# Kernel optimization log

Measured on AMD Instinct MI355X. Metric: run time of the kernel, lower is better.

## Reference

```python
import jax, jax.numpy as jnp
import numpy as np

N_NODES = 50000
N_EDGES = 800000
N_GRAPHS = 512


def gcn_conv(x, W, b, src, dst, n_nodes):
    # Standard PyG GCNConv: linear transform, add self-loops, D^-1/2 (A+I) D^-1/2 aggregation.
    x = x @ W  # [N, out]
    loop = jnp.arange(n_nodes, dtype=src.dtype)
    s = jnp.concatenate([src, loop])  # [E+N]
    d = jnp.concatenate([dst, loop])
    deg = jax.ops.segment_sum(jnp.ones_like(d, dtype=x.dtype), d, num_segments=n_nodes)
    dinv = jnp.where(deg > 0, jax.lax.rsqrt(jnp.maximum(deg, 1e-12)), 0.0)
    norm = dinv[s] * dinv[d]  # [E+N]
    msg = x[s] * norm[:, None]  # gather + scale
    out = jax.ops.segment_sum(msg, d, num_segments=n_nodes)  # scatter-add
    return out + b


def setup_inputs() -> dict:
    key = jax.random.key(0)
    ks = jax.random.split(key, 10)
    x = jax.random.normal(ks[0], (N_NODES, 128), dtype=jnp.float32)
    edge_index = jax.random.randint(ks[1], (2, N_EDGES), 0, N_NODES, dtype=jnp.int64)
    batch = jnp.sort(jax.random.randint(ks[2], (N_NODES,), 0, N_GRAPHS, dtype=jnp.int64))
    y = jax.random.randint(ks[3], (N_GRAPHS,), 0, 4, dtype=jnp.int64)
    W1 = jax.random.normal(ks[4], (128, 64), dtype=jnp.float32) * (1.0 / np.sqrt(128))
    b1 = jnp.zeros((64,), dtype=jnp.float32)
    W2 = jax.random.normal(ks[5], (64, 64), dtype=jnp.float32) * (1.0 / np.sqrt(64))
    b2 = jnp.zeros((64,), dtype=jnp.float32)
    Wfc = jax.random.normal(ks[6], (64, 4), dtype=jnp.float32) * (1.0 / np.sqrt(64))
    bfc = jnp.zeros((4,), dtype=jnp.float32)
    return {"x": x, "edge_index": edge_index, "batch": batch, "y": y,
            "W1": W1, "b1": b1, "W2": W2, "b2": b2, "Wfc": Wfc, "bfc": bfc}


def reference(x, edge_index, batch, y, W1, b1, W2, b2, Wfc, bfc):
    src, dst = edge_index[0], edge_index[1]
    h = jax.nn.relu(gcn_conv(x, W1, b1, src, dst, N_NODES))
    h = jax.nn.relu(gcn_conv(h, W2, b2, src, dst, N_NODES))
    # global mean pool over graph ids
    sums = jax.ops.segment_sum(h, batch, num_segments=N_GRAPHS)  # [G, out]
    cnts = jax.ops.segment_sum(jnp.ones((h.shape[0],), h.dtype), batch, num_segments=N_GRAPHS)
    pooled = sums / jnp.maximum(cnts, 1.0)[:, None]
    logits = pooled @ Wfc + bfc
    logp = jax.nn.log_softmax(logits, axis=1)
    return (logp, y)
```

## Files before the change

### kernel.cpp

```cpp
#include <hip/hip_runtime.h>
#include <hip/hip_fp16.h>
#include <math.h>

#define N_NODES 50000
#define N_EDGES 800000
#define N_GRAPHS 512
#define NBKT 196
#define SENT N_NODES
#define CAP_T 6144
#define CAP_S 8192

typedef float v2f __attribute__((ext_vector_type(2)));

#define OFF_BCNT    0u
#define OFF_DINV    1024u
#define OFF_OFFS2   201216u
#define OFF_TMP     601344u
#define OFF_SORTED  5418240u
#define OFF_XS8_1   11840768u
#define OFF_XS8_2   15041024u
#define OFF_H2      18241280u

__global__ __launch_bounds__(256) void binA(const int* __restrict__ src, const int* __restrict__ dst,
                                            int* __restrict__ bcnt, unsigned int* __restrict__ tmp,
                                            unsigned int* __restrict__ x1, unsigned int* __restrict__ x2) {
    __shared__ int cnt[256];
    __shared__ int lo[256];
    __shared__ int cnt2[256];
    __shared__ int baseg[256];
    __shared__ unsigned int ldsPK[4096];
    __shared__ int ldsDST[4096];
    int t = threadIdx.x;
    cnt[t] = 0; cnt2[t] = 0;
    if (blockIdx.x == 0) {
        if (t < 16) x1[N_NODES * 16 + t] = 0;
        else if (t < 32) x2[N_NODES * 16 + (t - 16)] = 0;
    }
    __syncthreads();
    int e0 = blockIdx.x * 4096;
    int nE = N_EDGES - e0; if (nE > 4096) nE = 4096;
    int sA[16], dA[16];
#pragma unroll
    for (int i = 0; i < 16; ++i) {
        int e = e0 + i * 256 + t;
        if (e < N_EDGES) {
            sA[i] = src[e];
            dA[i] = dst[e];
            atomicAdd(&cnt[dA[i] >> 8], 1);
        } else dA[i] = -1;
    }
    __syncthreads();
    {
        int v = cnt[t];
        lo[t] = v;
        __syncthreads();
        for (int d = 1; d < 256; d <<= 1) {
            int a = (t >= d) ? lo[t - d] : 0;
            __syncthreads();
            lo[t] += a;
            __syncthreads();
        }
        int ex = lo[t] - v;
        __syncthreads();
        lo[t] = ex;
        baseg[t] = (t < NBKT && v) ? atomicAdd(&bcnt[t], v) : 0;
    }
    __syncthreads();
#pragma unroll
    for (int i = 0; i < 16; ++i) {
        if (dA[i] >= 0) {
            int b = dA[i] >> 8;
            int pl = lo[b] + atomicAdd(&cnt2[b], 1);
            ldsPK[pl] = (unsigned int)sA[i] | ((unsigned int)(dA[i] & 255) << 17);
            ldsDST[pl] = b * CAP_T + baseg[b] + (pl - lo[b]);
        }
    }
    __syncthreads();
    for (int p = t; p < nE; p += 256)
        tmp[ldsDST[p]] = ldsPK[p];
}

__global__ __launch_bounds__(256) void binB2(const unsigned int* __restrict__ tmp,
                                             const int* __restrict__ bcnt,
                                             int* __restrict__ sorted, int2* __restrict__ offs2,
                                             float* __restrict__ dinv) {
    __shared__ int cnt[256];
    __shared__ int scn[256];
    __shared__ int cur[256];
    __shared__ int ldsS[CAP_S];
    int b = blockIdx.x, t = threadIdx.x;
    cnt[t] = 0;
    __syncthreads();
    int m = bcnt[b];
    const unsigned int* tp = tmp + b * CAP_T;
    for (int e = t; e < m; e += 256) atomicAdd(&cnt[tp[e] >> 17], 1);
    __syncthreads();
    int deg = cnt[t];
    int pdeg = (deg + 7) & ~7;
    scn[t] = pdeg;
    __syncthreads();
    for (int d = 1; d < 256; d <<= 1) {
        int a = (t >= d) ? scn[t - d] : 0;
        __syncthreads();
        scn[t] += a;
        __syncthreads();
    }
    int begl = scn[t] - pdeg;
    int ptot = scn[255];
    int node = b * 256 + t;
    if (node < N_NODES) {
        offs2[node] = make_int2(b * CAP_S + begl, b * CAP_S + begl + pdeg);
        dinv[node] = rsqrtf(1.0f + (float)deg);
    }
    cur[t] = begl;
    __syncthreads();
    for (int e = t; e < m; e += 256) {
        unsigned int pk = tp[e];
        int p = atomicAdd(&cur[pk >> 17], 1);
        ldsS[p] = (int)(pk & 0x1FFFFu);
    }
    __syncthreads();
    for (int p = cur[t]; p < begl + pdeg; ++p) ldsS[p] = SENT;
    __syncthreads();
    int4* dst4 = (int4*)(sorted + b * CAP_S);
    const int4* src4 = (const int4*)ldsS;
    for (int p = t; p < (ptot >> 2); p += 256) dst4[p] = src4[p];
}

__global__ __launch_bounds__(256) void gemm1(const float* __restrict__ X, const float* __restrict__ W,
                                             const float* __restrict__ dinv, unsigned int* __restrict__ xs8) {
    __shared__ float sW[128 * 64];
    __shared__ float sX[16 * 132];
    int tid = threadIdx.x;
    {
        const float4* ws = (const float4*)W;
        float4* wd = (float4*)sW;
        for (int i = tid; i < 2048; i += 256) wd[i] = ws[i];
    }
    int row0 = blockIdx.x * 16;
    {
        const float4* xs = (const float4*)(X + row0 * 128);
        for (int i = tid; i < 512; i += 256) {
            int r = i >> 5, q = i & 31;
            *(float4*)&sX[r * 132 + 4 * q] = xs[r * 32 + q];
        }
    }
    __syncthreads();
    int r = tid >> 4;
    int cg = (tid & 15) * 4;
    int row = row0 + r;
    float a0 = 0, a1 = 0, a2 = 0, a3 = 0;
#pragma unroll 8
    for (int k = 0; k < 128; ++k) {
        float xv = sX[r * 132 + k];
        float4 w = *(const float4*)&sW[k * 64 + cg];
        a0 += xv * w.x; a1 += xv * w.y; a2 += xv * w.z; a3 += xv * w.w;
    }
    float s = dinv[row];
    unsigned int pk = 0;
    pk = __builtin_amdgcn_cvt_pk_fp8_f32(a0 * s, a1 * s, pk, false);
    pk = __builtin_amdgcn_cvt_pk_fp8_f32(a2 * s, a3 * s, pk, true);
    xs8[row * 16 + (cg >> 2)] = pk;
}

#define ADD_ROW(rv) { \
    v2f f0 = __builtin_amdgcn_cvt_pk_f32_fp8((rv).x, false); \
    v2f f1 = __builtin_amdgcn_cvt_pk_f32_fp8((rv).x, true); \
    v2f f2 = __builtin_amdgcn_cvt_pk_f32_fp8((rv).y, false); \
    v2f f3 = __builtin_amdgcn_cvt_pk_f32_fp8((rv).y, true); \
    a0 += f0.x; a1 += f0.y; a2 += f1.x; a3 += f1.y; \
    a4 += f2.x; a5 += f2.y; a6 += f3.x; a7 += f3.y; }

#define RED_SUB() { \
    a0 += __shfl_xor(a0, 8);  a1 += __shfl_xor(a1, 8);  a2 += __shfl_xor(a2, 8);  a3 += __shfl_xor(a3, 8); \
    a4 += __shfl_xor(a4, 8);  a5 += __shfl_xor(a5, 8);  a6 += __shfl_xor(a6, 8);  a7 += __shfl_xor(a7, 8); \
    a0 += __shfl_xor(a0, 16); a1 += __shfl_xor(a1, 16); a2 += __shfl_xor(a2, 16); a3 += __shfl_xor(a3, 16); \
    a4 += __shfl_xor(a4, 16); a5 += __shfl_xor(a5, 16); a6 += __shfl_xor(a6, 16); a7 += __shfl_xor(a7, 16); \
    a0 += __shfl_xor(a0, 32); a1 += __shfl_xor(a1, 32); a2 += __shfl_xor(a2, 32); a3 += __shfl_xor(a3, 32); \
    a4 += __shfl_xor(a4, 32); a5 += __shfl_xor(a5, 32); a6 += __shfl_xor(a6, 32); a7 += __shfl_xor(a7, 32); }

#define GATHER_BODY(FLUSH_ADV) \
    int lane = threadIdx.x & 63; \
    int sub = lane >> 3, frag = lane & 7; \
    int n0 = wv * 4; \
    int2 oe = offs2[n0 + (lane < 4 ? lane : 3)]; \
    int e0 = __shfl(oe.x, 0), e1 = __shfl(oe.x, 1), e2 = __shfl(oe.x, 2); \
    int e3 = __shfl(oe.x, 3), e4 = __shfl(oe.y, 3); \
    int G   = (e4 - e0) >> 3; \
    int nb1 = (e1 - e0) >> 3, nb2 = (e2 - e0) >> 3, nb3 = (e3 - e0) >> 3; \
    const int* sb = sorted + e0 + sub; \
    int i0 = (0 < G) ? sb[0]  : SENT; \
    int i1 = (1 < G) ? sb[8]  : SENT; \
    int i2 = (2 < G) ? sb[16] : SENT; \
    int i3 = (3 < G) ? sb[24] : SENT; \
    float4 bA = *(const float4*)(bias + frag * 8); \
    float4 bB = *(const float4*)(bias + frag * 8 + 4); \
    int cur = 0; \
    uint2 sv = *(const uint2*)(xs8 + n0 * 64 + frag * 8); \
    float dv = dinv[n0]; \
    float a0 = 0, a1 = 0, a2 = 0, a3 = 0, a4 = 0, a5 = 0, a6 = 0, a7 = 0; \
    for (int g = 0; g < G; g += 4) { \
        uint2 r0 = *(const uint2*)(xs8 + i0 * 64 + frag * 8); \
        uint2 r1 = *(const uint2*)(xs8 + i1 * 64 + frag * 8); \
        uint2 r2 = *(const uint2*)(xs8 + i2 * 64 + frag * 8); \
        uint2 r3 = *(const uint2*)(xs8 + i3 * 64 + frag * 8); \
        const int* np = sb + (g + 4) * 8; \
        i0 = (g + 4 < G) ? np[0]  : SENT; \
        i1 = (g + 5 < G) ? np[8]  : SENT; \
        i2 = (g + 6 < G) ? np[16] : SENT; \
        i3 = (g + 7 < G) ? np[24] : SENT; \
        {   int gg = g; \
            int nxt = BND_NXT(); \
            while (cur < 4 && gg >= nxt) { FLUSH_ADV(); nxt = BND_NXT(); } \
            ADD_ROW(r0); } \
        if (g + 1 < G) { \
            int gg = g + 1; \
            int nxt = BND_NXT(); \
            while (cur < 4 && gg >= nxt) { FLUSH_ADV(); nxt = BND_NXT(); } \
            ADD_ROW(r1); \
        } \
        if (g + 2 < G) { \
            int gg = g + 2; \
            int nxt = BND_NXT(); \
            while (cur < 4 && gg >= nxt) { FLUSH_ADV(); nxt = BND_NXT(); } \
            ADD_ROW(r2); \
        } \
        if (g + 3 < G) { \
            int gg = g + 3; \
            int nxt = BND_NXT(); \
            while (cur < 4 && gg >= nxt) { FLUSH_ADV(); nxt = BND_NXT(); } \
            ADD_ROW(r3); \
        } \
    } \
    while (cur < 4) { FLUSH_ADV(); }

#define BND_NXT() (cur == 0 ? nb1 : cur == 1 ? nb2 : cur == 2 ? nb3 : G)

__global__ __launch_bounds__(256) void gather_fuse(const unsigned char* __restrict__ xs8,
                                                   const int2* __restrict__ offs2,
                                                   const int* __restrict__ sorted,
                                                   const float* __restrict__ dinv,
                                                   const float* __restrict__ bias,
                                                   const float* __restrict__ W2,
                                                   unsigned int* __restrict__ xs8o) {
    __shared__ float sW2[64 * 64];
    __shared__ float sH[16][64];
    {
        const float4* ws = (const float4*)W2;
        float4* wd = (float4*)sW2;
        for (int i = threadIdx.x; i < 1024; i += 256) wd[i] = ws[i];
    }
    int wvl = threadIdx.x >> 6;
    int wv = blockIdx.x * 4 + wvl;

#define FLUSH_LDS() { \
    if (sub == 0) ADD_ROW(sv); \
    RED_SUB(); \
    if (sub == 0) { \
        float4 w0, w1; \
        w0.x = fmaxf(a0 * dv + bA.x, 0.0f); w0.y = fmaxf(a1 * dv + bA.y, 0.0f); \
        w0.z = fmaxf(a2 * dv + bA.z, 0.0f); w0.w = fmaxf(a3 * dv + bA.w, 0.0f); \
        w1.x = fmaxf(a4 * dv + bB.x, 0.0f); w1.y = fmaxf(a5 * dv + bB.y, 0.0f); \
        w1.z = fmaxf(a6 * dv + bB.z, 0.0f); w1.w = fmaxf(a7 * dv + bB.w, 0.0f); \
        *(float4*)&sH[wvl * 4 + cur][frag * 8]     = w0; \
        *(float4*)&sH[wvl * 4 + cur][frag * 8 + 4] = w1; \
    } \
    a0 = a1 = a2 = a3 = a4 = a5 = a6 = a7 = 0.0f; \
    cur++; \
    if (cur < 4) { \
        sv = *(const uint2*)(xs8 + (n0 + cur) * 64 + frag * 8); \
        dv = dinv[n0 + cur]; \
    } }

    GATHER_BODY(FLUSH_LDS)
#undef FLUSH_LDS
    __syncthreads();
    int r = threadIdx.x >> 4;
    int cg = (threadIdx.x & 15) * 4;
    int node = blockIdx.x * 16 + r;
    float b0 = 0, b1 = 0, b2 = 0, b3 = 0;
#pragma unroll 8
    for (int k = 0; k < 64; ++k) {
        float hv = sH[r][k];
        float4 w = *(const float4*)&sW2[k * 64 + cg];
        b0 += hv * w.x; b1 += hv * w.y; b2 += hv * w.z; b3 += hv * w.w;
    }
    float s = dinv[node];
    unsigned int pk = 0;
    pk = __builtin_amdgcn_cvt_pk_fp8_f32(b0 * s, b1 * s, pk, false);
    pk = __builtin_amdgcn_cvt_pk_fp8_f32(b2 * s, b3 * s, pk, true);
    xs8o[node * 16 + (cg >> 2)] = pk;
}

__global__ __launch_bounds__(256) void gather_h2(const unsigned char* __restrict__ xs8,
                                                 const int2* __restrict__ offs2,
                                                 const int* __restrict__ sorted,
                                                 const float* __restrict__ dinv,
                                                 const float* __restrict__ bias,
                                                 __half* __restrict__ h2) {
    int wv = blockIdx.x * 4 + (threadIdx.x >> 6);

#define FLUSH_H2() { \
    if (sub == 0) ADD_ROW(sv); \
    RED_SUB(); \
    if (sub == 0) { \
        float v0 = fmaxf(a0 * dv + bA.x, 0.0f), v1 = fmaxf(a1 * dv + bA.y, 0.0f); \
        float v2 = fmaxf(a2 * dv + bA.z, 0.0f), v3 = fmaxf(a3 * dv + bA.w, 0.0f); \
        float v4 = fmaxf(a4 * dv + bB.x, 0.0f), v5 = fmaxf(a5 * dv + bB.y, 0.0f); \
        float v6 = fmaxf(a6 * dv + bB.z, 0.0f), v7 = fmaxf(a7 * dv + bB.w, 0.0f); \
        __half2 p0 = __floats2half2_rn(v0, v1), p1 = __floats2half2_rn(v2, v3); \
        __half2 p2 = __floats2half2_rn(v4, v5), p3 = __floats2half2_rn(v6, v7); \
        uint4 pk; \
        pk.x = *(unsigned int*)&p0; pk.y = *(unsigned int*)&p1; \
        pk.z = *(unsigned int*)&p2; pk.w = *(unsigned int*)&p3; \
        *(uint4*)(h2 + (n0 + cur) * 64 + frag * 8) = pk; \
    } \
    a0 = a1 = a2 = a3 = a4 = a5 = a6 = a7 = 0.0f; \
    cur++; \
    if (cur < 4) { \
        sv = *(const uint2*)(xs8 + (n0 + cur) * 64 + frag * 8); \
        dv = dinv[n0 + cur]; \
    } }

    GATHER_BODY(FLUSH_H2)
#undef FLUSH_H2
}

__device__ __forceinline__ int lower_bound(const int* __restrict__ a, int n, int v) {
    int lo = 0, hi = n;
    while (lo < hi) { int m = (lo + hi) >> 1; if (a[m] < v) lo = m + 1; else hi = m; }
    return lo;
}

__global__ __launch_bounds__(256) void pool_head(const __half* __restrict__ h2,
                                                 const int* __restrict__ batch,
                                                 const float* __restrict__ Wfc, const float* __restrict__ bfc,
                                                 const int* __restrict__ y, float* __restrict__ out) {
    __shared__ int s_beg, s_end;
    __shared__ float sh[4][64];
    __shared__ float pl[64];
    __shared__ float lg[4];
    int g = blockIdx.x;
    int t = threadIdx.x;
    if (t == 0) s_beg = lower_bound(batch, N_NODES, g);
    if (t == 1) s_end = lower_bound(batch, N_NODES, g + 1);
    __syncthreads();
    int beg = s_beg, end = s_end;
    int f = t & 63, seg = t >> 6;
    float s = 0.0f;
    for (int r = beg + seg; r < end; r += 4) s += __half2float(h2[r * 64 + f]);
    sh[seg][f] = s;
    __syncthreads();
    if (t < 64) {
        float p = sh[0][t] + sh[1][t] + sh[2][t] + sh[3][t];
        pl[t] = p / fmaxf((float)(end - beg), 1.0f);
    }
    __syncthreads();
    if (t < 4) {
        float l = bfc[t];
#pragma unroll
        for (int k = 0; k < 64; ++k) l += pl[k] * Wfc[k * 4 + t];
        lg[t] = l;
    }
    __syncthreads();
    if (t == 0) {
        float l0 = lg[0], l1 = lg[1], l2 = lg[2], l3 = lg[3];
        float m = fmaxf(fmaxf(l0, l1), fmaxf(l2, l3));
        float ss = expf(l0 - m) + expf(l1 - m) + expf(l2 - m) + expf(l3 - m);
        float lse = m + logf(ss);
        out[g * 4 + 0] = l0 - lse;
        out[g * 4 + 1] = l1 - lse;
        out[g * 4 + 2] = l2 - lse;
        out[g * 4 + 3] = l3 - lse;
        out[N_GRAPHS * 4 + g] = (float)y[g];
    }
}

extern "C" void kernel_launch(void* const* d_in, const int* in_sizes, int n_in,
                              void* d_out, int out_size, void* d_ws, size_t ws_size,
                              hipStream_t stream) {
    const float* x     = (const float*)d_in[0];
    const int*   ei    = (const int*)d_in[1];
    const int*   batch = (const int*)d_in[2];
    const int*   y     = (const int*)d_in[3];
    const float* W1    = (const float*)d_in[4];
    const float* b1    = (const float*)d_in[5];
    const float* W2    = (const float*)d_in[6];
    const float* b2    = (const float*)d_in[7];
    const float* Wfc   = (const float*)d_in[8];
    const float* bfc   = (const float*)d_in[9];
    float* out = (float*)d_out;

    const int* src = ei;
    const int* dst = ei + N_EDGES;

    char* wsb = (char*)d_ws;
    int*          bcnt   = (int*)(wsb + OFF_BCNT);
    float*        dinv   = (float*)(wsb + OFF_DINV);
    int2*         offs2  = (int2*)(wsb + OFF_OFFS2);
    unsigned int* tmp    = (unsigned int*)(wsb + OFF_TMP);
    int*          sorted = (int*)(wsb + OFF_SORTED);
    unsigned int* xs8_1  = (unsigned int*)(wsb + OFF_XS8_1);
    unsigned int* xs8_2  = (unsigned int*)(wsb + OFF_XS8_2);
    __half*       h2     = (__half*)(wsb + OFF_H2);

    hipMemsetAsync(bcnt, 0, 1024u, stream);

    binA<<<NBKT, 256, 0, stream>>>(src, dst, bcnt, tmp, xs8_1, xs8_2);
    binB2<<<NBKT, 256, 0, stream>>>(tmp, bcnt, sorted, offs2, dinv);

    gemm1<<<N_NODES / 16, 256, 0, stream>>>(x, W1, dinv, xs8_1);
    gather_fuse<<<N_NODES / 16, 256, 0, stream>>>((const unsigned char*)xs8_1, offs2, sorted,
                                                  dinv, b1, W2, xs8_2);
    gather_h2<<<N_NODES / 16, 256, 0, stream>>>((const unsigned char*)xs8_2, offs2, sorted,
                                                dinv, b2, h2);

    pool_head<<<N_GRAPHS, 256, 0, stream>>>(h2, batch, Wfc, bfc, y, out);
}
```

Baseline: 198.7 us.

## Interleave neighbor lists per 8-node group so each subgroup gathers one node

Changes the CSR layout so each group of 8 consecutive nodes stores its neighbor lists interleaved and padded to the group's max degree plus a self-loop entry. In the gather kernels each 8-lane subgroup now accumulates one node directly, which removes the cross-subgroup shuffle reductions and the per-edge boundary checks of the old 4-nodes-per-wave scheme. binA also uses twice as many blocks with 2048 edges each, and the fused GEMM now handles 32 rows per block. In exchange, degree imbalance inside a group adds padded sentinel loads, and the sorted buffer grows.

```diff
diff --git a/kernel.cpp b/kernel.cpp
--- a/kernel.cpp
+++ b/kernel.cpp
@@ -8,18 +8,22 @@
 #define NBKT 196
 #define SENT N_NODES
 #define CAP_T 6144
-#define CAP_S 8192
+#define CAP_S 12288
+#define EPB 2048
+#define NBLK_A 391
+#define N_GROUPS 6250
+#define NBLK_G 1563
 
 typedef float v2f __attribute__((ext_vector_type(2)));
 
 #define OFF_BCNT    0u
 #define OFF_DINV    1024u
-#define OFF_OFFS2   201216u
-#define OFF_TMP     601344u
-#define OFF_SORTED  5418240u
-#define OFF_XS8_1   11840768u
-#define OFF_XS8_2   15041024u
-#define OFF_H2      18241280u
+#define OFF_GGRP    201216u
+#define OFF_TMP     251392u
+#define OFF_SORTED  5068288u
+#define OFF_XS8_1   14702080u
+#define OFF_XS8_2   17902336u
+#define OFF_H2      21102592u
 
 __global__ __launch_bounds__(256) void binA(const int* __restrict__ src, const int* __restrict__ dst,
                                             int* __restrict__ bcnt, unsigned int* __restrict__ tmp,
@@ -28,8 +32,8 @@
     __shared__ int lo[256];
     __shared__ int cnt2[256];
     __shared__ int baseg[256];
-    __shared__ unsigned int ldsPK[4096];
-    __shared__ int ldsDST[4096];
+    __shared__ unsigned int ldsPK[EPB];
+    __shared__ int ldsDST[EPB];
     int t = threadIdx.x;
     cnt[t] = 0; cnt2[t] = 0;
     if (blockIdx.x == 0) {
@@ -37,11 +41,11 @@
         else if (t < 32) x2[N_NODES * 16 + (t - 16)] = 0;
     }
     __syncthreads();
-    int e0 = blockIdx.x * 4096;
-    int nE = N_EDGES - e0; if (nE > 4096) nE = 4096;
-    int sA[16], dA[16];
+    int e0 = blockIdx.x * EPB;
+    int nE = N_EDGES - e0; if (nE > EPB) nE = EPB;
+    int sA[8], dA[8];
 #pragma unroll
-    for (int i = 0; i < 16; ++i) {
+    for (int i = 0; i < 8; ++i) {
         int e = e0 + i * 256 + t;
         if (e < N_EDGES) {
             sA[i] = src[e];
@@ -67,7 +71,7 @@
     }
     __syncthreads();
 #pragma unroll
-    for (int i = 0; i < 16; ++i) {
+    for (int i = 0; i < 8; ++i) {
         if (dA[i] >= 0) {
             int b = dA[i] >> 8;
             int pl = lo[b] + atomicAdd(&cnt2[b], 1);
@@ -82,11 +86,13 @@
 
 __global__ __launch_bounds__(256) void binB2(const unsigned int* __restrict__ tmp,
                                              const int* __restrict__ bcnt,
-                                             int* __restrict__ sorted, int2* __restrict__ offs2,
+                                             int* __restrict__ sorted, int2* __restrict__ ggrp,
                                              float* __restrict__ dinv) {
     __shared__ int cnt[256];
-    __shared__ int scn[256];
+    __shared__ int lbs[256];
     __shared__ int cur[256];
+    __shared__ int gK[32];
+    __shared__ int gpre[33];
     __shared__ int ldsS[CAP_S];
     int b = blockIdx.x, t = threadIdx.x;
     cnt[t] = 0;
@@ -95,33 +101,43 @@
     const unsigned int* tp = tmp + b * CAP_T;
     for (int e = t; e < m; e += 256) atomicAdd(&cnt[tp[e] >> 17], 1);
     __syncthreads();
+    int node = b * 256 + t;
+    int real = node < N_NODES;
     int deg = cnt[t];
-    int pdeg = (deg + 7) & ~7;
-    scn[t] = pdeg;
-    __syncthreads();
-    for (int d = 1; d < 256; d <<= 1) {
-        int a = (t >= d) ? scn[t - d] : 0;
-        __syncthreads();
-        scn[t] += a;
-        __syncthreads();
-    }
-    int begl = scn[t] - pdeg;
-    int ptot = scn[255];
-    int node = b * 256 + t;
-    if (node < N_NODES) {
-        offs2[node] = make_int2(b * CAP_S + begl, b * CAP_S + begl + pdeg);
+    int count = real ? deg + 1 : 0;
+    int mx = count;
+    mx = max(mx, __shfl_xor(mx, 1));
+    mx = max(mx, __shfl_xor(mx, 2));
+    mx = max(mx, __shfl_xor(mx, 4));
+    int K = (mx + 3) & ~3;
+    int KP = K + 4;
+    if ((t & 7) == 0) gK[t >> 3] = KP;
+    __syncthreads();
+    if (t == 0) {
+        int s = 0;
+        for (int g = 0; g < 32; ++g) { gpre[g] = s; s += gK[g]; }
+        gpre[32] = s;
+    }
+    __syncthreads();
+    int lb = 8 * gpre[t >> 3] + (t & 7);
+    lbs[t] = lb;
+    cur[t] = real ? 1 : 0;
+    if (real) {
         dinv[node] = rsqrtf(1.0f + (float)deg);
-    }
-    cur[t] = begl;
+        ldsS[lb] = node;
+    }
+    if ((t & 7) == 0) ggrp[b * 32 + (t >> 3)] = make_int2(b * CAP_S + 8 * gpre[t >> 3], K);
     __syncthreads();
     for (int e = t; e < m; e += 256) {
         unsigned int pk = tp[e];
-        int p = atomicAdd(&cur[pk >> 17], 1);
-        ldsS[p] = (int)(pk & 0x1FFFFu);
-    }
-    __syncthreads();
-    for (int p = cur[t]; p < begl + pdeg; ++p) ldsS[p] = SENT;
-    __syncthreads();
+        int d = (int)(pk >> 17);
+        int j = atomicAdd(&cur[d], 1);
+        ldsS[lbs[d] + j * 8] = (int)(pk & 0x1FFFFu);
+    }
+    __syncthreads();
+    for (int j = cur[t]; j < KP; ++j) ldsS[lb + j * 8] = SENT;
+    __syncthreads();
+    int ptot = 8 * gpre[32];
     int4* dst4 = (int4*)(sorted + b * CAP_S);
     const int4* src4 = (const int4*)ldsS;
     for (int p = t; p < (ptot >> 2); p += 256) dst4[p] = src4[p];
@@ -171,159 +187,106 @@
     a0 += f0.x; a1 += f0.y; a2 += f1.x; a3 += f1.y; \
     a4 += f2.x; a5 += f2.y; a6 += f3.x; a7 += f3.y; }
 
-#define RED_SUB() { \
-    a0 += __shfl_xor(a0, 8);  a1 += __shfl_xor(a1, 8);  a2 += __shfl_xor(a2, 8);  a3 += __shfl_xor(a3, 8); \
-    a4 += __shfl_xor(a4, 8);  a5 += __shfl_xor(a5, 8);  a6 += __shfl_xor(a6, 8);  a7 += __shfl_xor(a7, 8); \
-    a0 += __shfl_xor(a0, 16); a1 += __shfl_xor(a1, 16); a2 += __shfl_xor(a2, 16); a3 += __shfl_xor(a3, 16); \
-    a4 += __shfl_xor(a4, 16); a5 += __shfl_xor(a5, 16); a6 += __shfl_xor(a6, 16); a7 += __shfl_xor(a7, 16); \
-    a0 += __shfl_xor(a0, 32); a1 += __shfl_xor(a1, 32); a2 += __shfl_xor(a2, 32); a3 += __shfl_xor(a3, 32); \
-    a4 += __shfl_xor(a4, 32); a5 += __shfl_xor(a5, 32); a6 += __shfl_xor(a6, 32); a7 += __shfl_xor(a7, 32); }
-
-#define GATHER_BODY(FLUSH_ADV) \
+#define GATHER_ACC() \
     int lane = threadIdx.x & 63; \
     int sub = lane >> 3, frag = lane & 7; \
-    int n0 = wv * 4; \
-    int2 oe = offs2[n0 + (lane < 4 ? lane : 3)]; \
-    int e0 = __shfl(oe.x, 0), e1 = __shfl(oe.x, 1), e2 = __shfl(oe.x, 2); \
-    int e3 = __shfl(oe.x, 3), e4 = __shfl(oe.y, 3); \
-    int G   = (e4 - e0) >> 3; \
-    int nb1 = (e1 - e0) >> 3, nb2 = (e2 - e0) >> 3, nb3 = (e3 - e0) >> 3; \
-    const int* sb = sorted + e0 + sub; \
-    int i0 = (0 < G) ? sb[0]  : SENT; \
-    int i1 = (1 < G) ? sb[8]  : SENT; \
-    int i2 = (2 < G) ? sb[16] : SENT; \
-    int i3 = (3 < G) ? sb[24] : SENT; \
-    float4 bA = *(const float4*)(bias + frag * 8); \
-    float4 bB = *(const float4*)(bias + frag * 8 + 4); \
-    int cur = 0; \
-    uint2 sv = *(const uint2*)(xs8 + n0 * 64 + frag * 8); \
-    float dv = dinv[n0]; \
+    int node = grp * 8 + sub; \
+    int2 gi = ggrp[grp]; \
+    int K = gi.y; \
+    const int* sp = sorted + gi.x + sub; \
+    const uint2* xr = (const uint2*)xs8 + frag; \
     float a0 = 0, a1 = 0, a2 = 0, a3 = 0, a4 = 0, a5 = 0, a6 = 0, a7 = 0; \
-    for (int g = 0; g < G; g += 4) { \
-        uint2 r0 = *(const uint2*)(xs8 + i0 * 64 + frag * 8); \
-        uint2 r1 = *(const uint2*)(xs8 + i1 * 64 + frag * 8); \
-        uint2 r2 = *(const uint2*)(xs8 + i2 * 64 + frag * 8); \
-        uint2 r3 = *(const uint2*)(xs8 + i3 * 64 + frag * 8); \
-        const int* np = sb + (g + 4) * 8; \
-        i0 = (g + 4 < G) ? np[0]  : SENT; \
-        i1 = (g + 5 < G) ? np[8]  : SENT; \
-        i2 = (g + 6 < G) ? np[16] : SENT; \
-        i3 = (g + 7 < G) ? np[24] : SENT; \
-        {   int gg = g; \
-            int nxt = BND_NXT(); \
-            while (cur < 4 && gg >= nxt) { FLUSH_ADV(); nxt = BND_NXT(); } \
-            ADD_ROW(r0); } \
-        if (g + 1 < G) { \
-            int gg = g + 1; \
-            int nxt = BND_NXT(); \
-            while (cur < 4 && gg >= nxt) { FLUSH_ADV(); nxt = BND_NXT(); } \
-            ADD_ROW(r1); \
-        } \
-        if (g + 2 < G) { \
-            int gg = g + 2; \
-            int nxt = BND_NXT(); \
-            while (cur < 4 && gg >= nxt) { FLUSH_ADV(); nxt = BND_NXT(); } \
-            ADD_ROW(r2); \
-        } \
-        if (g + 3 < G) { \
-            int gg = g + 3; \
-            int nxt = BND_NXT(); \
-            while (cur < 4 && gg >= nxt) { FLUSH_ADV(); nxt = BND_NXT(); } \
-            ADD_ROW(r3); \
-        } \
-    } \
-    while (cur < 4) { FLUSH_ADV(); }
-
-#define BND_NXT() (cur == 0 ? nb1 : cur == 1 ? nb2 : cur == 2 ? nb3 : G)
+    int i0 = sp[0], i1 = sp[8], i2 = sp[16], i3 = sp[24]; \
+    for (int k = 0; k < K; k += 4) { \
+        uint2 r0 = xr[i0 * 8]; \
+        uint2 r1 = xr[i1 * 8]; \
+        uint2 r2 = xr[i2 * 8]; \
+        uint2 r3 = xr[i3 * 8]; \
+        const int* np = sp + (k + 4) * 8; \
+        i0 = np[0]; i1 = np[8]; i2 = np[16]; i3 = np[24]; \
+        ADD_ROW(r0); ADD_ROW(r1); ADD_ROW(r2); ADD_ROW(r3); \
+    }
 
 __global__ __launch_bounds__(256) void gather_fuse(const unsigned char* __restrict__ xs8,
-                                                   const int2* __restrict__ offs2,
+                                                   const int2* __restrict__ ggrp,
                                                    const int* __restrict__ sorted,
                                                    const float* __restrict__ dinv,
                                                    const float* __restrict__ bias,
                                                    const float* __restrict__ W2,
                                                    unsigned int* __restrict__ xs8o) {
     __shared__ float sW2[64 * 64];
-    __shared__ float sH[16][64];
+    __shared__ float sH[32][68];
     {
         const float4* ws = (const float4*)W2;
         float4* wd = (float4*)sW2;
         for (int i = threadIdx.x; i < 1024; i += 256) wd[i] = ws[i];
     }
     int wvl = threadIdx.x >> 6;
-    int wv = blockIdx.x * 4 + wvl;
-
-#define FLUSH_LDS() { \
-    if (sub == 0) ADD_ROW(sv); \
-    RED_SUB(); \
-    if (sub == 0) { \
-        float4 w0, w1; \
-        w0.x = fmaxf(a0 * dv + bA.x, 0.0f); w0.y = fmaxf(a1 * dv + bA.y, 0.0f); \
-        w0.z = fmaxf(a2 * dv + bA.z, 0.0f); w0.w = fmaxf(a3 * dv + bA.w, 0.0f); \
-        w1.x = fmaxf(a4 * dv + bB.x, 0.0f); w1.y = fmaxf(a5 * dv + bB.y, 0.0f); \
-        w1.z = fmaxf(a6 * dv + bB.z, 0.0f); w1.w = fmaxf(a7 * dv + bB.w, 0.0f); \
-        *(float4*)&sH[wvl * 4 + cur][frag * 8]     = w0; \
-        *(float4*)&sH[wvl * 4 + cur][frag * 8 + 4] = w1; \
-    } \
-    a0 = a1 = a2 = a3 = a4 = a5 = a6 = a7 = 0.0f; \
-    cur++; \
-    if (cur < 4) { \
-        sv = *(const uint2*)(xs8 + (n0 + cur) * 64 + frag * 8); \
-        dv = dinv[n0 + cur]; \
-    } }
-
-    GATHER_BODY(FLUSH_LDS)
-#undef FLUSH_LDS
-    __syncthreads();
-    int r = threadIdx.x >> 4;
-    int cg = (threadIdx.x & 15) * 4;
-    int node = blockIdx.x * 16 + r;
-    float b0 = 0, b1 = 0, b2 = 0, b3 = 0;
+    int grp = blockIdx.x * 4 + wvl;
+
+    GATHER_ACC()
+
+    {
+        float dv = dinv[node];
+        float4 bA = *(const float4*)(bias + frag * 8);
+        float4 bB = *(const float4*)(bias + frag * 8 + 4);
+        float4 w0, w1;
+        w0.x = fmaxf(a0 * dv + bA.x, 0.0f); w0.y = fmaxf(a1 * dv + bA.y, 0.0f);
+        w0.z = fmaxf(a2 * dv + bA.z, 0.0f); w0.w = fmaxf(a3 * dv + bA.w, 0.0f);
+        w1.x = fmaxf(a4 * dv + bB.x, 0.0f); w1.y = fmaxf(a5 * dv + bB.y, 0.0f);
+        w1.z = fmaxf(a6 * dv + bB.z, 0.0f); w1.w = fmaxf(a7 * dv + bB.w, 0.0f);
+        *(float4*)&sH[wvl * 8 + sub][frag * 8] = w0;
+        *(float4*)&sH[wvl * 8 + sub][frag * 8 + 4] = w1;
+    }
+    __syncthreads();
+    int r = threadIdx.x >> 3;
+    int cg = (threadIdx.x & 7) * 8;
+    float b0 = 0, b1 = 0, b2 = 0, b3 = 0, b4 = 0, b5 = 0, b6 = 0, b7 = 0;
 #pragma unroll 8
     for (int k = 0; k < 64; ++k) {
         float hv = sH[r][k];
-        float4 w = *(const float4*)&sW2[k * 64 + cg];
-        b0 += hv * w.x; b1 += hv * w.y; b2 += hv * w.z; b3 += hv * w.w;
-    }
-    float s = dinv[node];
-    unsigned int pk = 0;
-    pk = __builtin_amdgcn_cvt_pk_fp8_f32(b0 * s, b1 * s, pk, false);
-    pk = __builtin_amdgcn_cvt_pk_fp8_f32(b2 * s, b3 * s, pk, true);
-    xs8o[node * 16 + (cg >> 2)] = pk;
+        float4 wa = *(const float4*)&sW2[k * 64 + cg];
+        float4 wb = *(const float4*)&sW2[k * 64 + cg + 4];
+        b0 += hv * wa.x; b1 += hv * wa.y; b2 += hv * wa.z; b3 += hv * wa.w;
+        b4 += hv * wb.x; b5 += hv * wb.y; b6 += hv * wb.z; b7 += hv * wb.w;
+    }
+    int node2 = blockIdx.x * 32 + r;
+    if (node2 < N_NODES) {
+        float s = dinv[node2];
+        unsigned int p0 = 0, p1 = 0;
+        p0 = __builtin_amdgcn_cvt_pk_fp8_f32(b0 * s, b1 * s, p0, false);
+        p0 = __builtin_amdgcn_cvt_pk_fp8_f32(b2 * s, b3 * s, p0, true);
+        p1 = __builtin_amdgcn_cvt_pk_fp8_f32(b4 * s, b5 * s, p1, false);
+        p1 = __builtin_amdgcn_cvt_pk_fp8_f32(b6 * s, b7 * s, p1, true);
+        *(uint2*)(xs8o + node2 * 16 + (cg >> 2)) = make_uint2(p0, p1);
+    }
 }
 
 __global__ __launch_bounds__(256) void gather_h2(const unsigned char* __restrict__ xs8,
-                                                 const int2* __restrict__ offs2,
+                                                 const int2* __restrict__ ggrp,
                                                  const int* __restrict__ sorted,
                                                  const float* __restrict__ dinv,
                                                  const float* __restrict__ bias,
                                                  __half* __restrict__ h2) {
-    int wv = blockIdx.x * 4 + (threadIdx.x >> 6);
-
-#define FLUSH_H2() { \
-    if (sub == 0) ADD_ROW(sv); \
-    RED_SUB(); \
-    if (sub == 0) { \
-        float v0 = fmaxf(a0 * dv + bA.x, 0.0f), v1 = fmaxf(a1 * dv + bA.y, 0.0f); \
-        float v2 = fmaxf(a2 * dv + bA.z, 0.0f), v3 = fmaxf(a3 * dv + bA.w, 0.0f); \
-        float v4 = fmaxf(a4 * dv + bB.x, 0.0f), v5 = fmaxf(a5 * dv + bB.y, 0.0f); \
-        float v6 = fmaxf(a6 * dv + bB.z, 0.0f), v7 = fmaxf(a7 * dv + bB.w, 0.0f); \
-        __half2 p0 = __floats2half2_rn(v0, v1), p1 = __floats2half2_rn(v2, v3); \
-        __half2 p2 = __floats2half2_rn(v4, v5), p3 = __floats2half2_rn(v6, v7); \
-        uint4 pk; \
-        pk.x = *(unsigned int*)&p0; pk.y = *(unsigned int*)&p1; \
-        pk.z = *(unsigned int*)&p2; pk.w = *(unsigned int*)&p3; \
-        *(uint4*)(h2 + (n0 + cur) * 64 + frag * 8) = pk; \
-    } \
-    a0 = a1 = a2 = a3 = a4 = a5 = a6 = a7 = 0.0f; \
-    cur++; \
-    if (cur < 4) { \
-        sv = *(const uint2*)(xs8 + (n0 + cur) * 64 + frag * 8); \
-        dv = dinv[n0 + cur]; \
-    } }
-
-    GATHER_BODY(FLUSH_H2)
-#undef FLUSH_H2
+    int grp = blockIdx.x * 4 + (threadIdx.x >> 6);
+
+    GATHER_ACC()
+
+    if (node < N_NODES) {
+        float dv = dinv[node];
+        float4 bA = *(const float4*)(bias + frag * 8);
+        float4 bB = *(const float4*)(bias + frag * 8 + 4);
+        float v0 = fmaxf(a0 * dv + bA.x, 0.0f), v1 = fmaxf(a1 * dv + bA.y, 0.0f);
+        float v2 = fmaxf(a2 * dv + bA.z, 0.0f), v3 = fmaxf(a3 * dv + bA.w, 0.0f);
+        float v4 = fmaxf(a4 * dv + bB.x, 0.0f), v5 = fmaxf(a5 * dv + bB.y, 0.0f);
+        float v6 = fmaxf(a6 * dv + bB.z, 0.0f), v7 = fmaxf(a7 * dv + bB.w, 0.0f);
+        __half2 p0 = __floats2half2_rn(v0, v1), p1 = __floats2half2_rn(v2, v3);
+        __half2 p2 = __floats2half2_rn(v4, v5), p3 = __floats2half2_rn(v6, v7);
+        uint4 pk;
+        pk.x = *(unsigned int*)&p0; pk.y = *(unsigned int*)&p1;
+        pk.z = *(unsigned int*)&p2; pk.w = *(unsigned int*)&p3;
+        *(uint4*)(h2 + node * 64 + frag * 8) = pk;
+    }
 }
 
 __device__ __forceinline__ int lower_bound(const int* __restrict__ a, int n, int v) {
@@ -397,7 +360,7 @@
     char* wsb = (char*)d_ws;
     int*          bcnt   = (int*)(wsb + OFF_BCNT);
     float*        dinv   = (float*)(wsb + OFF_DINV);
-    int2*         offs2  = (int2*)(wsb + OFF_OFFS2);
+    int2*         ggrp   = (int2*)(wsb + OFF_GGRP);
     unsigned int* tmp    = (unsigned int*)(wsb + OFF_TMP);
     int*          sorted = (int*)(wsb + OFF_SORTED);
     unsigned int* xs8_1  = (unsigned int*)(wsb + OFF_XS8_1);
@@ -406,14 +369,14 @@
 
     hipMemsetAsync(bcnt, 0, 1024u, stream);
 
-    binA<<<NBKT, 256, 0, stream>>>(src, dst, bcnt, tmp, xs8_1, xs8_2);
-    binB2<<<NBKT, 256, 0, stream>>>(tmp, bcnt, sorted, offs2, dinv);
+    binA<<<NBLK_A, 256, 0, stream>>>(src, dst, bcnt, tmp, xs8_1, xs8_2);
+    binB2<<<NBKT, 256, 0, stream>>>(tmp, bcnt, sorted, ggrp, dinv);
 
     gemm1<<<N_NODES / 16, 256, 0, stream>>>(x, W1, dinv, xs8_1);
-    gather_fuse<<<N_NODES / 16, 256, 0, stream>>>((const unsigned char*)xs8_1, offs2, sorted,
-                                                  dinv, b1, W2, xs8_2);
-    gather_h2<<<N_NODES / 16, 256, 0, stream>>>((const unsigned char*)xs8_2, offs2, sorted,
-                                                dinv, b2, h2);
+    gather_fuse<<<NBLK_G, 256, 0, stream>>>((const unsigned char*)xs8_1, ggrp, sorted,
+                                            dinv, b1, W2, xs8_2);
+    gather_h2<<<NBLK_G, 256, 0, stream>>>((const unsigned char*)xs8_2, ggrp, sorted,
+                                          dinv, b2, h2);
 
     pool_head<<<N_GRAPHS, 256, 0, stream>>>(h2, batch, Wfc, bfc, y, out);
 }
```

Measured after the change: 198.0 us. No clear change (-0.4%).
